# Kernel tuning notes

Hardware: AMD Instinct MI355X
Metric: run time of the kernel (lower is better)

## Reference

```python
import jax, jax.numpy as jnp
import numpy as np

N_E = 8192
E_DIM = 256
BETA = 1.0


def setup_inputs() -> dict:
    key = jax.random.key(0)
    k1, k2 = jax.random.split(key)
    z = jax.random.normal(k1, (16, E_DIM, 32, 32), dtype=jnp.float32)
    # torch init: uniform(-1/n_e, 1/n_e)
    emb_w = jax.random.uniform(k2, (N_E, E_DIM), dtype=jnp.float32,
                               minval=-1.0 / N_E, maxval=1.0 / N_E)
    return {"z": z, "emb_w": emb_w}


def reference(z, emb_w):
    # z: [B, C, H, W] -> [B, H, W, C]
    z_nhwc = jnp.transpose(z, (0, 2, 3, 1))
    B, H, W, C = z_nhwc.shape
    z_flat = z_nhwc.reshape(-1, C)  # [N, e_dim]

    # squared euclidean distances: ||z||^2 + ||e||^2 - 2 z e^T  -> [N, n_e]
    d = (jnp.sum(z_flat ** 2, axis=1, keepdims=True)
         + jnp.sum(emb_w ** 2, axis=1)[None, :]
         - 2.0 * jnp.matmul(z_flat, emb_w.T))

    min_idx = jnp.argmin(d, axis=1)  # [N]
    z_q = emb_w[min_idx].reshape(B, H, W, C)

    sg = jax.lax.stop_gradient
    loss = (BETA * jnp.mean((sg(z_q) - z_nhwc) ** 2)
            + jnp.mean((z_q - sg(z_nhwc)) ** 2))

    # straight-through estimator
    z_q = z_nhwc + sg(z_q - z_nhwc)
    z_q = jnp.transpose(z_q, (0, 3, 1, 2))  # back to [B, C, H, W]
    min_idx = min_idx.reshape(B, H, W)
    return z_q, loss, min_idx
```

## Files before the change

kernel.cpp:

```cpp
#include <hip/hip_runtime.h>
#include <hip/hip_fp16.h>
#include <float.h>

#define K_DIM 256
#define HW1 1024
#define NROWS 16384
#define NCODES 8192

typedef __attribute__((ext_vector_type(8))) short bf16x8;
typedef __attribute__((ext_vector_type(4))) float f32x4;

__device__ __forceinline__ ushort bf16rn(float x) {
    unsigned u = __float_as_uint(x);
    return (ushort)((u + 0x7FFFu + ((u >> 16) & 1u)) >> 16);
}

__device__ __forceinline__ void gl16(const void* g, void* l) {
    __builtin_amdgcn_global_load_lds((const __attribute__((address_space(1))) void*)g,
                                     (__attribute__((address_space(3))) void*)l, 16, 0, 0);
}

__global__ __launch_bounds__(256) void k_cvt(const float* __restrict__ z,
                                             float* __restrict__ zf32,
                                             ushort* __restrict__ z16,
                                             float* __restrict__ zn,
                                             const float* __restrict__ emb,
                                             ushort* __restrict__ e16,
                                             unsigned* __restrict__ gcnt,
                                             float* __restrict__ loss) {
    __shared__ float ls[32 * 260];
    const int blk = blockIdx.x;
    const int t = threadIdx.x;
    if (blk >= 512) {
        const int eb = blk - 512;
        if (eb == 0) {
            gcnt[t] = 0u;
            if (t == 0) *loss = 0.f;
        }
#pragma unroll
        for (int i = 0; i < 8; ++i) {
            int f4 = eb * 2048 + i * 256 + t;
            float4 v = *(const float4*)(emb + (size_t)f4 * 4);
            ushort4 h;
            h.x = bf16rn(v.x); h.y = bf16rn(v.y);
            h.z = bf16rn(v.z); h.w = bf16rn(v.w);
            *(ushort4*)(e16 + (size_t)f4 * 4) = h;
        }
        return;
    }
    const int b = blk >> 5, hw0 = (blk & 31) * 32;
    const float* src = z + (size_t)b * 262144 + hw0;
#pragma unroll
    for (int i = 0; i < 2; ++i) {
        int m = t + i * 256;
        int kq = m >> 3, hq = m & 7;
        const float* s0 = src + (size_t)(kq * 4) * 1024 + hq * 4;
        float4 r0 = *(const float4*)(s0);
        float4 r1 = *(const float4*)(s0 + 1024);
        float4 r2 = *(const float4*)(s0 + 2048);
        float4 r3 = *(const float4*)(s0 + 3072);
        *(float4*)(ls + (hq * 4 + 0) * 260 + kq * 4) = make_float4(r0.x, r1.x, r2.x, r3.x);
        *(float4*)(ls + (hq * 4 + 1) * 260 + kq * 4) = make_float4(r0.y, r1.y, r2.y, r3.y);
        *(float4*)(ls + (hq * 4 + 2) * 260 + kq * 4) = make_float4(r0.z, r1.z, r2.z, r3.z);
        *(float4*)(ls + (hq * 4 + 3) * 260 + kq * 4) = make_float4(r0.w, r1.w, r2.w, r3.w);
    }
    __syncthreads();
    {
        const int w = t >> 6, cl = t & 63;
#pragma unroll
        for (int i = 0; i < 8; ++i) {
            int r = i * 4 + w;
            float4 v = *(const float4*)(ls + r * 260 + cl * 4);
            int n = b * 1024 + hw0 + r;
            *(float4*)(zf32 + (size_t)n * 256 + cl * 4) = v;
            ushort4 h;
            h.x = bf16rn(v.x); h.y = bf16rn(v.y);
            h.z = bf16rn(v.z); h.w = bf16rn(v.w);
            *(ushort4*)(z16 + (size_t)n * 256 + cl * 4) = h;
        }
    }
    if (t < 32) {
        const float* lr = ls + t * 260;
        float half[2];
#pragma unroll
        for (int h = 0; h < 2; ++h) {
            float rj[8];
            {
                float4 a = *(const float4*)(lr + h * 128);
                float4 b4 = *(const float4*)(lr + h * 128 + 4);
                float s;
                s = a.x * a.x; asm volatile("" : "+v"(s)); rj[0] = s;
                s = a.y * a.y; asm volatile("" : "+v"(s)); rj[1] = s;
                s = a.z * a.z; asm volatile("" : "+v"(s)); rj[2] = s;
                s = a.w * a.w; asm volatile("" : "+v"(s)); rj[3] = s;
                s = b4.x * b4.x; asm volatile("" : "+v"(s)); rj[4] = s;
                s = b4.y * b4.y; asm volatile("" : "+v"(s)); rj[5] = s;
                s = b4.z * b4.z; asm volatile("" : "+v"(s)); rj[6] = s;
                s = b4.w * b4.w; asm volatile("" : "+v"(s)); rj[7] = s;
            }
#pragma unroll
            for (int i = 1; i < 16; ++i) {
                float4 a = *(const float4*)(lr + h * 128 + 8 * i);
                float4 b4 = *(const float4*)(lr + h * 128 + 8 * i + 4);
                float s;
                s = a.x * a.x; asm volatile("" : "+v"(s)); rj[0] += s;
                s = a.y * a.y; asm volatile("" : "+v"(s)); rj[1] += s;
                s = a.z * a.z; asm volatile("" : "+v"(s)); rj[2] += s;
                s = a.w * a.w; asm volatile("" : "+v"(s)); rj[3] += s;
                s = b4.x * b4.x; asm volatile("" : "+v"(s)); rj[4] += s;
                s = b4.y * b4.y; asm volatile("" : "+v"(s)); rj[5] += s;
                s = b4.z * b4.z; asm volatile("" : "+v"(s)); rj[6] += s;
                s = b4.w * b4.w; asm volatile("" : "+v"(s)); rj[7] += s;
            }
            half[h] = ((rj[0] + rj[1]) + (rj[2] + rj[3])) +
                      ((rj[4] + rj[5]) + (rj[6] + rj[7]));
        }
        zn[b * 1024 + hw0 + t] = half[0] + half[1];
    }
}

__global__ __launch_bounds__(256) void k_coarse(
    const ushort* __restrict__ z16, const ushort* __restrict__ e16,
    ushort* __restrict__ tbl) {
    __shared__ char smem[35840];
    char* As = smem;
    char* Bs = smem + 16384;
    float* parts = (float*)smem;
    ushort* tb = (ushort*)(smem + 34816);
    const int tid = threadIdx.x;
    const int w = tid >> 6, lane = tid & 63;
    const int tx = lane & 15, q = lane >> 4;
    const int row0 = blockIdx.x * 128, c0 = blockIdx.y * 128;
    const int Am = (w & 1) * 64, Bn = (w >> 1) * 64;

    f32x4 acc[4][4];
#pragma unroll
    for (int mi = 0; mi < 4; ++mi)
#pragma unroll
        for (int ni = 0; ni < 4; ++ni) acc[mi][ni] = (f32x4){0.f, 0.f, 0.f, 0.f};

    for (int k0 = 0; k0 < K_DIM; k0 += 64) {
#pragma unroll
        for (int j = 0; j < 4; ++j) {
            int r = (w * 4 + j) * 8 + (lane >> 3);
            int c = (lane & 7) ^ (r & 7);
            gl16(z16 + (((size_t)(row0 + r)) << 8) + k0 + (c << 3),
                 As + (w * 4 + j) * 1024);
            gl16(e16 + (((size_t)(c0 + r)) << 8) + k0 + (c << 3),
                 Bs + (w * 4 + j) * 1024);
        }
        __syncthreads();
#pragma unroll
        for (int ks = 0; ks < 2; ++ks) {
            int cd = ks * 4;
            bf16x8 af[4], bfv[4];
#pragma unroll
            for (int mi = 0; mi < 4; ++mi)
                af[mi] = *(const bf16x8*)(As + (Am + mi * 16 + tx) * 128 +
                                          (((cd + q) ^ (tx & 7)) << 4));
#pragma unroll
            for (int ni = 0; ni < 4; ++ni)
                bfv[ni] = *(const bf16x8*)(Bs + (Bn + ni * 16 + tx) * 128 +
                                           (((cd + q) ^ (tx & 7)) << 4));
#pragma unroll
            for (int mi = 0; mi < 4; ++mi)
#pragma unroll
                for (int ni = 0; ni < 4; ++ni)
                    acc[mi][ni] = __builtin_amdgcn_mfma_f32_16x16x32_bf16(
                        af[mi], bfv[ni], acc[mi][ni], 0, 0, 0);
        }
        __syncthreads();
    }

#pragma unroll
    for (int g = 0; g < 2; ++g) {
        int gb = (w >> 1) * 2 + g;
#pragma unroll
        for (int mi = 0; mi < 4; ++mi) {
#pragma unroll
            for (int e = 0; e < 4; ++e) {
                float pm = fmaxf(acc[mi][2 * g][e], acc[mi][2 * g + 1][e]);
                int row = Am + mi * 16 + q * 4 + e;
                parts[(gb * 128 + row) * 17 + tx] = pm;
            }
        }
    }
    __syncthreads();
#pragma unroll
    for (int r2 = 0; r2 < 2; ++r2) {
        int p = tid * 2 + r2;
        const float* pr = parts + p * 17;
        float f0 = fmaxf(pr[0], pr[1]), f1 = fmaxf(pr[2], pr[3]);
        float f2 = fmaxf(pr[4], pr[5]), f3 = fmaxf(pr[6], pr[7]);
        float f4 = fmaxf(pr[8], pr[9]), f5 = fmaxf(pr[10], pr[11]);
        float f6 = fmaxf(pr[12], pr[13]), f7 = fmaxf(pr[14], pr[15]);
        float m = fmaxf(fmaxf(fmaxf(f0, f1), fmaxf(f2, f3)),
                        fmaxf(fmaxf(f4, f5), fmaxf(f6, f7)));
        tb[(p & 127) * 4 + (p >> 7)] = __half_as_ushort(__float2half(m));
    }
    __syncthreads();
    if (tid < 128) {
        ushort4 v = *(ushort4*)(tb + tid * 4);
        *(ushort4*)(tbl + (size_t)(row0 + tid) * 256 + blockIdx.y * 4) = v;
    }
}

__global__ void k_flag(const ushort* __restrict__ tbl, ushort* __restrict__ bucket,
                       unsigned* __restrict__ gcnt,
                       unsigned long long* __restrict__ best) {
    const int wid = threadIdx.x >> 6, lane = threadIdx.x & 63;
    const int n = blockIdx.x * 4 + wid;
    if (lane == 0) best[n] = 0xFFFFFFFFFFFFFFFFull;
    ushort4 raw = *(const ushort4*)(tbl + (size_t)n * 256 + lane * 4);
    float gm[4];
    gm[0] = __half2float(__ushort_as_half(raw.x));
    gm[1] = __half2float(__ushort_as_half(raw.y));
    gm[2] = __half2float(__ushort_as_half(raw.z));
    gm[3] = __half2float(__ushort_as_half(raw.w));
    float gmax = fmaxf(fmaxf(gm[0], gm[1]), fmaxf(gm[2], gm[3]));
#pragma unroll
    for (int m = 1; m < 64; m <<= 1) gmax = fmaxf(gmax, __shfl_xor(gmax, m, 64));
    const float th = gmax - 1.0e-4f;
#pragma unroll
    for (int i = 0; i < 4; ++i) {
        if (gm[i] >= th) {
            int g = lane * 4 + i;
            unsigned pos = atomicAdd(&gcnt[g], 1u);
            bucket[(size_t)g * NROWS + pos] = (ushort)n;
        }
    }
}

__global__ __launch_bounds__(256) void k_rescore2(
    const float* __restrict__ zf32, const float* __restrict__ emb,
    const float* __restrict__ zn, const ushort* __restrict__ bucket,
    const unsigned* __restrict__ gcnt, unsigned long long* __restrict__ best) {
    __shared__ float eg[32 * 257];
    __shared__ float zs[8][256];
    __shared__ ushort rid[8];
    __shared__ float arow[8];
    const int g = blockIdx.x >> 2;
    const int split = blockIdx.x & 3;
    const int t = threadIdx.x;
    const int cnt = (int)gcnt[g];
    if (split * 8 >= cnt) return;
#pragma unroll
    for (int i = 0; i < 8; ++i) {
        int f = t + i * 256;
        int c = f >> 6, k4 = f & 63;
        float4 v = *(const float4*)(emb + (size_t)(g * 32 + c) * 256 + k4 * 4);
        float* dst = eg + c * 257 + k4 * 4;
        dst[0] = v.x; dst[1] = v.y; dst[2] = v.z; dst[3] = v.w;
    }
    for (int base = split * 8; base < cnt; base += 32) {
        __syncthreads();
        if (t < 8) {
            int i = base + t;
            if (i < cnt) {
                ushort r = bucket[(size_t)g * NROWS + i];
                rid[t] = r;
                arow[t] = zn[r];
            } else {
                rid[t] = 0xFFFF;
            }
        }
        __syncthreads();
#pragma unroll
        for (int i = 0; i < 2; ++i) {
            int f = t + i * 256;
            int s = f >> 6, k4 = f & 63;
            if (rid[s] != 0xFFFF)
                *(float4*)(&zs[s][k4 * 4]) =
                    *(const float4*)(zf32 + (size_t)rid[s] * 256 + k4 * 4);
        }
        __syncthreads();
        const int lane = t & 63, w = t >> 6;
        const int slot = w * 2 + (lane >> 5);
        const int code = lane & 31;
        if (rid[slot] != 0xFFFF) {
            const float* zr = zs[slot];
            const float* er = eg + code * 257;
            float acc = 0.f;
#pragma unroll 8
            for (int k = 0; k < 256; ++k) acc = fmaf(zr[k], er[k], acc);
            float d = arow[slot] - 2.f * acc;
            unsigned fb = __float_as_uint(d);
            fb ^= (fb & 0x80000000u) ? 0xFFFFFFFFu : 0x80000000u;
            unsigned long long pk =
                ((unsigned long long)fb << 32) | (unsigned)(g * 32 + code);
#pragma unroll
            for (int m = 1; m < 32; m <<= 1) {
                unsigned long long o = __shfl_xor(pk, m, 64);
                if (o < pk) pk = o;
            }
            if ((lane & 31) == 0) atomicMin(&best[rid[slot]], pk);
        }
    }
}

__global__ __launch_bounds__(256) void k_gather(
    const float* __restrict__ z, const float* __restrict__ emb,
    const unsigned long long* __restrict__ best, float* __restrict__ zq,
    float* __restrict__ oidx, float* __restrict__ loss) {
    __shared__ float eg[64][257];
    __shared__ float lsum[4];
    const int t = threadIdx.x;
    const int n0 = blockIdx.x * 64;
    const int b = n0 >> 10, hw0 = n0 & 1023;
    {
        const int row = t >> 2;
        const int cbase = (t & 3) * 64;
        const int code = (int)(unsigned)(best[n0 + row] & 0xFFFFFFFFull);
        if ((t & 3) == 0) oidx[n0 + row] = (float)code;
        const float* er = emb + (size_t)code * 256 + cbase;
        float* dst = &eg[row][cbase];
#pragma unroll
        for (int i = 0; i < 16; ++i) {
            float4 v = *(const float4*)(er + i * 4);
            dst[i * 4 + 0] = v.x; dst[i * 4 + 1] = v.y;
            dst[i * 4 + 2] = v.z; dst[i * 4 + 3] = v.w;
        }
    }
    __syncthreads();
    const int w = t >> 6, lane = t & 63;
    float acc = 0.f;
    const size_t obase = (size_t)b * 262144 + hw0 + lane;
#pragma unroll 4
    for (int ci = 0; ci < 64; ++ci) {
        int c = w * 64 + ci;
        float e = eg[lane][c];
        size_t off = obase + (size_t)c * 1024;
        float zv = z[off];
        zq[off] = e;
        float d = e - zv;
        acc = fmaf(d, d, acc);
    }
#pragma unroll
    for (int m = 32; m; m >>= 1) acc += __shfl_xor(acc, m, 64);
    if (lane == 0) lsum[w] = acc;
    __syncthreads();
    if (t == 0) {
        float s = (lsum[0] + lsum[1]) + (lsum[2] + lsum[3]);
        atomicAdd(loss, s * (2.f / 4194304.f));
    }
}

extern "C" void kernel_launch(void* const* d_in, const int* in_sizes, int n_in,
                              void* d_out, int out_size, void* d_ws, size_t ws_size,
                              hipStream_t stream) {
    const float* z = (const float*)d_in[0];
    const float* emb = (const float*)d_in[1];
    float* out = (float*)d_out;
    float* zq = out;
    float* loss = out + 4194304;
    float* oidx = out + 4194305;
    float* zf32 = out;

    ushort* z16 = (ushort*)d_ws;
    ushort* e16 = z16 + 4194304;
    ushort* tbl = e16 + 2097152;
    float* zn = (float*)(tbl + 4194304);
    unsigned long long* best = (unsigned long long*)(zn + 16384);
    unsigned* gcnt = (unsigned*)(best + 16384);
    ushort* bucket = z16;

    k_cvt<<<dim3(768), dim3(256), 0, stream>>>(z, zf32, z16, zn, emb, e16, gcnt, loss);
    k_coarse<<<dim3(NROWS / 128, NCODES / 128), dim3(256), 0, stream>>>(z16, e16, tbl);
    k_flag<<<dim3(NROWS / 4), dim3(256), 0, stream>>>(tbl, bucket, gcnt, best);
    k_rescore2<<<dim3(1024), dim3(256), 0, stream>>>(zf32, emb, zn, bucket, gcnt, best);
    k_gather<<<dim3(NROWS / 64), dim3(256), 0, stream>>>(z, emb, best, zq, oidx, loss);
}
```

Baseline: 234.3 us.

## Enlarge coarse GEMM tile to 256x256 with double-buffered LDS pipeline

Rewrites the coarse bf16 distance GEMM to use 256x256 output tiles with 512 threads and 128 KB of dynamic LDS. Global-to-LDS loads for the next K slice are issued between phased fragment reads and MFMA bursts, using explicit barriers, waitcnts and raised wave priority around the MFMAs. The goal is better data reuse and overlap of loads with compute. The per-32-code max reduction now stages fp16 partials and writes eight group maxima per row. The large LDS footprint limits occupancy to about one block per CU, and correctness depends on hand-placed waitcnt counts.

```diff
diff --git a/kernel.cpp b/kernel.cpp
--- a/kernel.cpp
+++ b/kernel.cpp
@@ -119,89 +119,152 @@
     }
 }
 
-__global__ __launch_bounds__(256) void k_coarse(
+__device__ __forceinline__ void stage_half(const ushort* __restrict__ g, char* l, int tid) {
+#pragma unroll
+    for (int i = 0; i < 2; ++i) {
+        int idx = i * 512 + tid;
+        int rl = idx >> 3;
+        int ck = (idx & 7) ^ (rl & 7);
+        gl16(g + (size_t)rl * 256 + ck * 8, l + idx * 16);
+    }
+}
+
+template <int MH, int NP>
+static __device__ __forceinline__ void ph_reads(const char* A, const char* B,
+                                                int arb, int brb, int swz0, int swz1,
+                                                bf16x8 Af[4][2], bf16x8 Bf[2][2]) {
+    if (NP == 0) {
+#pragma unroll
+        for (int mi = 0; mi < 4; ++mi) {
+            Af[mi][0] = *(const bf16x8*)(A + arb + (MH * 4 + mi) * 2048 + swz0);
+            Af[mi][1] = *(const bf16x8*)(A + arb + (MH * 4 + mi) * 2048 + swz1);
+        }
+    }
+#pragma unroll
+    for (int ni = 0; ni < 2; ++ni) {
+        Bf[ni][0] = *(const bf16x8*)(B + brb + (NP * 2 + ni) * 2048 + swz0);
+        Bf[ni][1] = *(const bf16x8*)(B + brb + (NP * 2 + ni) * 2048 + swz1);
+    }
+}
+
+template <int MH, int NP>
+static __device__ __forceinline__ void ph_mfma(bf16x8 Af[4][2], bf16x8 Bf[2][2],
+                                               f32x4 acc[8][4]) {
+    __builtin_amdgcn_s_setprio(1);
+#pragma unroll
+    for (int mi = 0; mi < 4; ++mi)
+#pragma unroll
+        for (int ni = 0; ni < 2; ++ni) {
+            f32x4 c = acc[MH * 4 + mi][NP * 2 + ni];
+            c = __builtin_amdgcn_mfma_f32_16x16x32_bf16(Af[mi][0], Bf[ni][0], c, 0, 0, 0);
+            c = __builtin_amdgcn_mfma_f32_16x16x32_bf16(Af[mi][1], Bf[ni][1], c, 0, 0, 0);
+            acc[MH * 4 + mi][NP * 2 + ni] = c;
+        }
+    __builtin_amdgcn_s_setprio(0);
+}
+
+#define BAR() __builtin_amdgcn_s_barrier()
+#define LGKM0() asm volatile("s_waitcnt lgkmcnt(0)" ::: "memory")
+
+__global__ __launch_bounds__(512, 2) void k_coarse(
     const ushort* __restrict__ z16, const ushort* __restrict__ e16,
     ushort* __restrict__ tbl) {
-    __shared__ char smem[35840];
-    char* As = smem;
-    char* Bs = smem + 16384;
-    float* parts = (float*)smem;
-    ushort* tb = (ushort*)(smem + 34816);
+    extern __shared__ char smem[];
     const int tid = threadIdx.x;
     const int w = tid >> 6, lane = tid & 63;
+    const int wm = w >> 2, wn = w & 3;
     const int tx = lane & 15, q = lane >> 4;
-    const int row0 = blockIdx.x * 128, c0 = blockIdx.y * 128;
-    const int Am = (w & 1) * 64, Bn = (w >> 1) * 64;
-
-    f32x4 acc[4][4];
-#pragma unroll
-    for (int mi = 0; mi < 4; ++mi)
+    const int tx7 = tx & 7;
+    const int row0 = blockIdx.x * 256, c0 = blockIdx.y * 256;
+    const ushort* Ag = z16 + (size_t)row0 * 256;
+    const ushort* Bg = e16 + (size_t)c0 * 256;
+    const int arb = (wm * 128 + tx) * 128;
+    const int brb = (wn * 64 + tx) * 128;
+    const int swz0 = ((q ^ tx7) << 4);
+    const int swz1 = (((4 + q) ^ tx7) << 4);
+
+    f32x4 acc[8][4];
+#pragma unroll
+    for (int mi = 0; mi < 8; ++mi)
 #pragma unroll
         for (int ni = 0; ni < 4; ++ni) acc[mi][ni] = (f32x4){0.f, 0.f, 0.f, 0.f};
-
-    for (int k0 = 0; k0 < K_DIM; k0 += 64) {
-#pragma unroll
-        for (int j = 0; j < 4; ++j) {
-            int r = (w * 4 + j) * 8 + (lane >> 3);
-            int c = (lane & 7) ^ (r & 7);
-            gl16(z16 + (((size_t)(row0 + r)) << 8) + k0 + (c << 3),
-                 As + (w * 4 + j) * 1024);
-            gl16(e16 + (((size_t)(c0 + r)) << 8) + k0 + (c << 3),
-                 Bs + (w * 4 + j) * 1024);
-        }
-        __syncthreads();
-#pragma unroll
-        for (int ks = 0; ks < 2; ++ks) {
-            int cd = ks * 4;
-            bf16x8 af[4], bfv[4];
-#pragma unroll
-            for (int mi = 0; mi < 4; ++mi)
-                af[mi] = *(const bf16x8*)(As + (Am + mi * 16 + tx) * 128 +
-                                          (((cd + q) ^ (tx & 7)) << 4));
-#pragma unroll
-            for (int ni = 0; ni < 4; ++ni)
-                bfv[ni] = *(const bf16x8*)(Bs + (Bn + ni * 16 + tx) * 128 +
-                                           (((cd + q) ^ (tx & 7)) << 4));
-#pragma unroll
-            for (int mi = 0; mi < 4; ++mi)
-#pragma unroll
-                for (int ni = 0; ni < 4; ++ni)
-                    acc[mi][ni] = __builtin_amdgcn_mfma_f32_16x16x32_bf16(
-                        af[mi], bfv[ni], acc[mi][ni], 0, 0, 0);
-        }
-        __syncthreads();
-    }
-
-#pragma unroll
-    for (int g = 0; g < 2; ++g) {
-        int gb = (w >> 1) * 2 + g;
-#pragma unroll
-        for (int mi = 0; mi < 4; ++mi) {
+    bf16x8 Af[4][2], Bf[2][2];
+
+    stage_half(Ag, smem, tid);
+    stage_half(Ag + (size_t)128 * 256, smem + 16384, tid);
+    stage_half(Bg, smem + 32768, tid);
+    stage_half(Bg + (size_t)128 * 256, smem + 49152, tid);
+    stage_half(Ag + 64, smem + 65536, tid);
+    stage_half(Ag + (size_t)128 * 256 + 64, smem + 81920, tid);
+    asm volatile("s_waitcnt vmcnt(4)" ::: "memory");
+    BAR();
+
+#pragma unroll
+    for (int t = 0; t < 4; ++t) {
+        const char* A = smem + (t & 1) * 65536;
+        const char* B = A + 32768;
+        char* nb = smem + ((t + 1) & 1) * 65536;
+        char* cb = smem + (t & 1) * 65536;
+
+        ph_reads<0, 0>(A, B, arb, brb, swz0, swz1, Af, Bf);
+        if (t < 3) stage_half(Bg + (t + 1) * 64, nb + 32768, tid);
+        BAR(); LGKM0();
+        ph_mfma<0, 0>(Af, Bf, acc);
+        BAR();
+
+        ph_reads<0, 1>(A, B, arb, brb, swz0, swz1, Af, Bf);
+        if (t < 3) stage_half(Bg + (size_t)128 * 256 + (t + 1) * 64, nb + 49152, tid);
+        BAR(); LGKM0();
+        ph_mfma<0, 1>(Af, Bf, acc);
+        BAR();
+
+        ph_reads<1, 0>(A, B, arb, brb, swz0, swz1, Af, Bf);
+        BAR(); LGKM0();
+        ph_mfma<1, 0>(Af, Bf, acc);
+        BAR();
+
+        ph_reads<1, 1>(A, B, arb, brb, swz0, swz1, Af, Bf);
+        if (t < 2) {
+            stage_half(Ag + (t + 2) * 64, cb, tid);
+            stage_half(Ag + (size_t)128 * 256 + (t + 2) * 64, cb + 16384, tid);
+            asm volatile("s_waitcnt vmcnt(4)" ::: "memory");
+        } else if (t == 2) {
+            asm volatile("s_waitcnt vmcnt(0)" ::: "memory");
+        }
+        BAR(); LGKM0();
+        ph_mfma<1, 1>(Af, Bf, acc);
+        BAR();
+    }
+
+    __syncthreads();
+    ushort* parts = (ushort*)smem;
+    ushort* tb = (ushort*)(smem + 98304);
+#pragma unroll
+    for (int mi = 0; mi < 8; ++mi)
+#pragma unroll
+        for (int g = 0; g < 2; ++g) {
+            int grp = wn * 2 + g;
 #pragma unroll
             for (int e = 0; e < 4; ++e) {
                 float pm = fmaxf(acc[mi][2 * g][e], acc[mi][2 * g + 1][e]);
-                int row = Am + mi * 16 + q * 4 + e;
-                parts[(gb * 128 + row) * 17 + tx] = pm;
+                int row = wm * 128 + mi * 16 + q * 4 + e;
+                parts[(grp * 256 + row) * 17 + tx] = __half_as_ushort(__float2half(pm));
             }
         }
-    }
-    __syncthreads();
-#pragma unroll
-    for (int r2 = 0; r2 < 2; ++r2) {
-        int p = tid * 2 + r2;
-        const float* pr = parts + p * 17;
-        float f0 = fmaxf(pr[0], pr[1]), f1 = fmaxf(pr[2], pr[3]);
-        float f2 = fmaxf(pr[4], pr[5]), f3 = fmaxf(pr[6], pr[7]);
-        float f4 = fmaxf(pr[8], pr[9]), f5 = fmaxf(pr[10], pr[11]);
-        float f6 = fmaxf(pr[12], pr[13]), f7 = fmaxf(pr[14], pr[15]);
-        float m = fmaxf(fmaxf(fmaxf(f0, f1), fmaxf(f2, f3)),
-                        fmaxf(fmaxf(f4, f5), fmaxf(f6, f7)));
-        tb[(p & 127) * 4 + (p >> 7)] = __half_as_ushort(__float2half(m));
-    }
-    __syncthreads();
-    if (tid < 128) {
-        ushort4 v = *(ushort4*)(tb + tid * 4);
-        *(ushort4*)(tbl + (size_t)(row0 + tid) * 256 + blockIdx.y * 4) = v;
+    __syncthreads();
+#pragma unroll
+    for (int j = 0; j < 4; ++j) {
+        int p = tid * 4 + j;
+        const ushort* pr = parts + p * 17;
+        float m = __half2float(__ushort_as_half(pr[0]));
+#pragma unroll
+        for (int i = 1; i < 16; ++i) m = fmaxf(m, __half2float(__ushort_as_half(pr[i])));
+        tb[(p & 255) * 8 + (p >> 8)] = __half_as_ushort(__float2half(m));
+    }
+    __syncthreads();
+    if (tid < 256) {
+        uint4 v = *(const uint4*)(tb + tid * 8);
+        *(uint4*)(tbl + (size_t)(row0 + tid) * 256 + blockIdx.y * 8) = v;
     }
 }
 
@@ -365,7 +428,7 @@
     ushort* bucket = z16;
 
     k_cvt<<<dim3(768), dim3(256), 0, stream>>>(z, zf32, z16, zn, emb, e16, gcnt, loss);
-    k_coarse<<<dim3(NROWS / 128, NCODES / 128), dim3(256), 0, stream>>>(z16, e16, tbl);
+    k_coarse<<<dim3(NROWS / 256, NCODES / 256), dim3(512), 131072, stream>>>(z16, e16, tbl);
     k_flag<<<dim3(NROWS / 4), dim3(256), 0, stream>>>(tbl, bucket, gcnt, best);
     k_rescore2<<<dim3(1024), dim3(256), 0, stream>>>(zf32, emb, zn, bucket, gcnt, best);
     k_gather<<<dim3(NROWS / 64), dim3(256), 0, stream>>>(z, emb, best, zq, oidx, loss);
```

Measured after the change: 250.9 us. 1.07x slower.
